# Optimization experiments

Measured on AMD Instinct MI355X. Metric: run time of the kernel, lower is better.

The kernel has to match this reference:

```python
import jax, jax.numpy as jnp
import numpy as np

LOW_THRESH = 0.3   # below -> background (label 0)
HIGH_THRESH = 0.7  # at/above -> foreground (label 1); in-between -> ignore (-1)


def _make_boxes(key, n):
    # two random corners per box -> valid (y1,x1,y2,x2) via min/max
    c = jax.random.uniform(key, (n, 2, 2), dtype=jnp.float32)
    lo = jnp.min(c, axis=1)
    hi = jnp.max(c, axis=1)
    return jnp.concatenate([lo, hi], axis=-1)  # [n, 4] = (y1, x1, y2, x2)


def setup_inputs() -> dict:
    key = jax.random.key(0)
    k1, k2 = jax.random.split(key)
    boxes1 = _make_boxes(k1, 262144)  # anchors / proposals
    boxes2 = _make_boxes(k2, 128)     # ground-truth boxes
    return {"boxes1": boxes1, "boxes2": boxes2}


def pairwise_iou(boxes1, boxes2):
    # boxes: (y1, x1, y2, x2). Result: [N1, N2]
    area1 = (boxes1[:, 2] - boxes1[:, 0]) * (boxes1[:, 3] - boxes1[:, 1])  # [N1]
    area2 = (boxes2[:, 2] - boxes2[:, 0]) * (boxes2[:, 3] - boxes2[:, 1])  # [N2]
    # intersection corners, broadcast [N1,1] vs [N2]
    iy1 = jnp.maximum(boxes1[:, None, 0], boxes2[None, :, 0])
    ix1 = jnp.maximum(boxes1[:, None, 1], boxes2[None, :, 1])
    iy2 = jnp.minimum(boxes1[:, None, 2], boxes2[None, :, 2])
    ix2 = jnp.minimum(boxes1[:, None, 3], boxes2[None, :, 3])
    inter = jnp.maximum(iy2 - iy1, 0.0) * jnp.maximum(ix2 - ix1, 0.0)  # [N1, N2]
    union = area1[:, None] + area2[None, :] - inter
    return inter / jnp.maximum(union, 1e-10)


def reference(boxes1, boxes2):
    iou = pairwise_iou(boxes1, boxes2)          # [N1, N2]
    matched_vals = jnp.max(iou, axis=1)         # [N1] best IoU per anchor
    matched_idx = jnp.argmax(iou, axis=1)       # [N1] index of best gt box
    labels = jnp.where(
        matched_vals >= HIGH_THRESH,
        jnp.int32(1),
        jnp.where(matched_vals < LOW_THRESH, jnp.int32(0), jnp.int32(-1)),
    )
    return matched_vals, matched_idx, labels
```

## Files before the change

### kernel.cpp

```cpp
#include <hip/hip_runtime.h>

#define N2 128
#define BLOCK 256

__global__ __launch_bounds__(BLOCK) void matcher_kernel(
    const float4* __restrict__ boxes1,
    const float4* __restrict__ boxes2,
    float* __restrict__ out_vals,
    float* __restrict__ out_idx,
    float* __restrict__ out_labels,
    int n1)
{
#pragma clang fp contract(off)
    __shared__ float4 s_b2[N2];
    __shared__ float s_area2[N2];

    const int t = threadIdx.x;
    if (t < N2) {
        float4 b = boxes2[t];
        s_b2[t] = b;
        s_area2[t] = (b.z - b.x) * (b.w - b.y);
    }
    __syncthreads();

    const int i = blockIdx.x * BLOCK + t;
    if (i >= n1) return;

    const float4 a = boxes1[i];
    const float area1 = (a.z - a.x) * (a.w - a.y);

    float best = -1.0f;
    int bidx = 0;

#pragma unroll 4
    for (int j = 0; j < N2; ++j) {
        const float4 b = s_b2[j];
        const float iy1 = fmaxf(a.x, b.x);
        const float ix1 = fmaxf(a.y, b.y);
        const float iy2 = fminf(a.z, b.z);
        const float ix2 = fminf(a.w, b.w);
        const float hy = fmaxf(iy2 - iy1, 0.0f);
        const float hx = fmaxf(ix2 - ix1, 0.0f);
        const float inter = hy * hx;
        const float uni = (area1 + s_area2[j]) - inter;
        const float iou = inter / fmaxf(uni, 1e-10f);
        if (iou > best) { best = iou; bidx = j; }
    }

    out_vals[i]   = best;
    out_idx[i]    = (float)bidx;
    out_labels[i] = (best >= 0.7f) ? 1.0f : ((best < 0.3f) ? 0.0f : -1.0f);
}

extern "C" void kernel_launch(void* const* d_in, const int* in_sizes, int n_in,
                              void* d_out, int out_size, void* d_ws, size_t ws_size,
                              hipStream_t stream) {
    const float4* boxes1 = (const float4*)d_in[0];
    const float4* boxes2 = (const float4*)d_in[1];
    const int n1 = in_sizes[0] / 4;

    float* out = (float*)d_out;
    float* out_vals   = out;
    float* out_idx    = out + n1;
    float* out_labels = out + 2 * n1;

    const int grid = (n1 + BLOCK - 1) / BLOCK;
    matcher_kernel<<<grid, BLOCK, 0, stream>>>(boxes1, boxes2,
                                               out_vals, out_idx, out_labels, n1);
}
```

Measured before the change: 31.70 us.

## Replace per-pair division with cross-multiplied IoU comparison and exact fallback

Instead of dividing inter by union for every pair, the kernel keeps the best (inter, union) fraction and compares candidates by cross-multiplication, doing a single division at the end. Two independent running maxima over the halves of the GT boxes shorten the dependency chain. When a comparison lands within a rounding tolerance band, a flag forces an exact recomputation with divisions so argmax ties and rounding match the reference. This adds extra multiplies and comparisons and a divergent slow path for near-ties.

```diff
diff --git a/kernel.cpp b/kernel.cpp
--- a/kernel.cpp
+++ b/kernel.cpp
@@ -2,6 +2,9 @@
 
 #define N2 128
 #define BLOCK 256
+
+#define ONE_P 1.00000095367431640625f
+#define ONE_M 0.99999904632568359375f
 
 __global__ __launch_bounds__(BLOCK) void matcher_kernel(
     const float4* __restrict__ boxes1,
@@ -29,27 +32,77 @@
     const float4 a = boxes1[i];
     const float area1 = (a.z - a.x) * (a.w - a.y);
 
-    float best = -1.0f;
-    int bidx = 0;
+    float biA = -1.0f, buA = 1.0f; int bxA = 0;
+    float biB = -1.0f, buB = 1.0f; int bxB = 64;
+    bool slow = false;
+
+#define FRAC(J, INTER, UM)                                            \
+    {                                                                 \
+        const float4 b = s_b2[(J)];                                   \
+        const float iy1 = fmaxf(a.x, b.x);                            \
+        const float ix1 = fmaxf(a.y, b.y);                            \
+        const float iy2 = fminf(a.z, b.z);                            \
+        const float ix2 = fminf(a.w, b.w);                            \
+        const float hy = fmaxf(iy2 - iy1, 0.0f);                      \
+        const float hx = fmaxf(ix2 - ix1, 0.0f);                      \
+        INTER = hy * hx;                                              \
+        UM = fmaxf((area1 + s_area2[(J)]) - INTER, 1e-10f);           \
+    }
+
+#define STEP(BI, BU, BX, INTER, UM, J)                                \
+    {                                                                 \
+        const float p1 = (INTER) * (BU);                              \
+        const float p2 = (BI) * (UM);                                 \
+        const float p2p = p2 * ONE_P;                                 \
+        const float p2m = p2 * ONE_M;                                 \
+        const bool upd = p1 > p2p;                                    \
+        slow = slow | (((INTER) > 0.0f) & (p1 >= p2m) & (p1 <= p2p)); \
+        if (upd) { BI = (INTER); BU = (UM); BX = (J); }               \
+    }
 
 #pragma unroll 4
-    for (int j = 0; j < N2; ++j) {
-        const float4 b = s_b2[j];
-        const float iy1 = fmaxf(a.x, b.x);
-        const float ix1 = fmaxf(a.y, b.y);
-        const float iy2 = fminf(a.z, b.z);
-        const float ix2 = fminf(a.w, b.w);
-        const float hy = fmaxf(iy2 - iy1, 0.0f);
-        const float hx = fmaxf(ix2 - ix1, 0.0f);
-        const float inter = hy * hx;
-        const float uni = (area1 + s_area2[j]) - inter;
-        const float iou = inter / fmaxf(uni, 1e-10f);
-        if (iou > best) { best = iou; bidx = j; }
+    for (int j = 0; j < 64; ++j) {
+        {
+            float inter, um;
+            FRAC(j, inter, um)
+            STEP(biA, buA, bxA, inter, um, j)
+        }
+        {
+            float inter, um;
+            FRAC(j + 64, inter, um)
+            STEP(biB, buB, bxB, inter, um, j + 64)
+        }
     }
 
-    out_vals[i]   = best;
-    out_idx[i]    = (float)bidx;
-    out_labels[i] = (best >= 0.7f) ? 1.0f : ((best < 0.3f) ? 0.0f : -1.0f);
+    {
+        const float p1 = biB * buA;
+        const float p2 = biA * buB;
+        const float p2p = p2 * ONE_P;
+        const float p2m = p2 * ONE_M;
+        const bool upd = p1 > p2p;
+        slow = slow | ((biB > 0.0f) & (p1 >= p2m) & (p1 <= p2p));
+        if (upd) { biA = biB; buA = buB; bxA = bxB; }
+    }
+
+    float d = biA / buA;
+    int xi = bxA;
+
+    if (slow) {
+        float best = -1.0f;
+        int bidx = 0;
+        for (int j = 0; j < N2; ++j) {
+            float inter, um;
+            FRAC(j, inter, um)
+            const float q = inter / um;
+            if (q > best) { best = q; bidx = j; }
+        }
+        d = best;
+        xi = bidx;
+    }
+
+    out_vals[i]   = d;
+    out_idx[i]    = (float)xi;
+    out_labels[i] = (d >= 0.7f) ? 1.0f : ((d < 0.3f) ? 0.0f : -1.0f);
 }
 
 extern "C" void kernel_launch(void* const* d_in, const int* in_sizes, int n_in,
```

After: 40.24 us. +26.9%, slower.

## Split gt-box loop across four wavefronts per anchor group and reduce in LDS

Applied to the files above, without the earlier changes.

Each block now handles 64 anchors, with each of its four wavefronts scanning 32 of the 128 ground-truth boxes. The partial argmax results are merged through shared memory. The gt box coordinates are read via wave-uniform global (scalar) loads instead of LDS, and launch bounds request more occupancy. The grid is four times larger, and the split adds a barrier plus a serial merge in one wavefront. Tie-breaking still keeps the first index, because waves are merged in ascending order with a strict greater-than.

```diff
diff --git a/kernel.cpp b/kernel.cpp
--- a/kernel.cpp
+++ b/kernel.cpp
@@ -2,8 +2,9 @@
 
 #define N2 128
 #define BLOCK 256
+#define APB 64
 
-__global__ __launch_bounds__(BLOCK) void matcher_kernel(
+__global__ __launch_bounds__(BLOCK, 8) void matcher_kernel(
     const float4* __restrict__ boxes1,
     const float4* __restrict__ boxes2,
     float* __restrict__ out_vals,
@@ -12,29 +13,34 @@
     int n1)
 {
 #pragma clang fp contract(off)
-    __shared__ float4 s_b2[N2];
     __shared__ float s_area2[N2];
+    __shared__ float s_q[4][APB];
+    __shared__ int   s_ix[4][APB];
 
     const int t = threadIdx.x;
     if (t < N2) {
-        float4 b = boxes2[t];
-        s_b2[t] = b;
+        const float4 b = boxes2[t];
         s_area2[t] = (b.z - b.x) * (b.w - b.y);
     }
     __syncthreads();
 
-    const int i = blockIdx.x * BLOCK + t;
-    if (i >= n1) return;
+    const int w    = __builtin_amdgcn_readfirstlane(t >> 6);
+    const int lane = t & 63;
+    const int i    = blockIdx.x * APB + lane;
+    const bool valid = (i < n1);
 
-    const float4 a = boxes1[i];
+    const float4 a = boxes1[valid ? i : 0];
     const float area1 = (a.z - a.x) * (a.w - a.y);
 
     float best = -1.0f;
-    int bidx = 0;
+    int   bidx = 0;
 
-#pragma unroll 4
-    for (int j = 0; j < N2; ++j) {
-        const float4 b = s_b2[j];
+    const int j0 = w * 32;
+#pragma unroll 8
+    for (int k = 0; k < 32; ++k) {
+        const int j = j0 + k;
+        const float4 b = boxes2[j];
+        const float a2 = s_area2[j];
         const float iy1 = fmaxf(a.x, b.x);
         const float ix1 = fmaxf(a.y, b.y);
         const float iy2 = fminf(a.z, b.z);
@@ -42,14 +48,30 @@
         const float hy = fmaxf(iy2 - iy1, 0.0f);
         const float hx = fmaxf(ix2 - ix1, 0.0f);
         const float inter = hy * hx;
-        const float uni = (area1 + s_area2[j]) - inter;
-        const float iou = inter / fmaxf(uni, 1e-10f);
-        if (iou > best) { best = iou; bidx = j; }
+        const float uni = (area1 + a2) - inter;
+        const float q = inter / fmaxf(uni, 1e-10f);
+        if (q > best) { best = q; bidx = j; }
     }
 
-    out_vals[i]   = best;
-    out_idx[i]    = (float)bidx;
-    out_labels[i] = (best >= 0.7f) ? 1.0f : ((best < 0.3f) ? 0.0f : -1.0f);
+    s_q[w][lane]  = best;
+    s_ix[w][lane] = bidx;
+    __syncthreads();
+
+    if (t < APB) {
+        const int ii = blockIdx.x * APB + t;
+        if (ii < n1) {
+            float q  = s_q[0][t];
+            int   ix = s_ix[0][t];
+#pragma unroll
+            for (int w2 = 1; w2 < 4; ++w2) {
+                const float q2 = s_q[w2][t];
+                if (q2 > q) { q = q2; ix = s_ix[w2][t]; }
+            }
+            out_vals[ii]   = q;
+            out_idx[ii]    = (float)ix;
+            out_labels[ii] = (q >= 0.7f) ? 1.0f : ((q < 0.3f) ? 0.0f : -1.0f);
+        }
+    }
 }
 
 extern "C" void kernel_launch(void* const* d_in, const int* in_sizes, int n_in,
@@ -64,7 +86,7 @@
     float* out_idx    = out + n1;
     float* out_labels = out + 2 * n1;
 
-    const int grid = (n1 + BLOCK - 1) / BLOCK;
+    const int grid = (n1 + APB - 1) / APB;
     matcher_kernel<<<grid, BLOCK, 0, stream>>>(boxes1, boxes2,
                                                out_vals, out_idx, out_labels, n1);
 }
```

Result: faster. 29.02 us (-8.5%).

## Use fast reciprocal IoU scan with top-2 tracking and exact fallback

Applied to the files above, without the earlier changes.

Replaces the per-pair IEEE division with a hardware approximate reciprocal and tracks the top two IoU values across two interleaved 64-wide chains. When the top two are within a relative band, it reruns the exact division scan so the argmax stays correct, then recomputes the winning IoU exactly for output. Ground-truth boxes are now read through uniform global loads instead of shared memory, and a launch-bounds occupancy hint is added. The cost is extra registers and a divergent fallback path for near-ties, with first-index tie-breaking handled through the fallback.

```diff
diff --git a/kernel.cpp b/kernel.cpp
--- a/kernel.cpp
+++ b/kernel.cpp
@@ -2,8 +2,9 @@
 
 #define N2 128
 #define BLOCK 256
+#define BAND 9.5367431640625e-07f
 
-__global__ __launch_bounds__(BLOCK) void matcher_kernel(
+__global__ __launch_bounds__(BLOCK, 8) void matcher_kernel(
     const float4* __restrict__ boxes1,
     const float4* __restrict__ boxes2,
     float* __restrict__ out_vals,
@@ -12,44 +13,87 @@
     int n1)
 {
 #pragma clang fp contract(off)
-    __shared__ float4 s_b2[N2];
     __shared__ float s_area2[N2];
 
     const int t = threadIdx.x;
     if (t < N2) {
-        float4 b = boxes2[t];
-        s_b2[t] = b;
+        const float4 b = boxes2[t];
         s_area2[t] = (b.z - b.x) * (b.w - b.y);
     }
     __syncthreads();
 
     const int i = blockIdx.x * BLOCK + t;
-    if (i >= n1) return;
-
-    const float4 a = boxes1[i];
+    const float4 a = boxes1[(i < n1) ? i : 0];
     const float area1 = (a.z - a.x) * (a.w - a.y);
 
-    float best = -1.0f;
-    int bidx = 0;
+    float bqA = -1.0f, b2A = -1.0f; int ixA = 0;
+    float bqB = -1.0f, b2B = -1.0f; int ixB = 0;
 
 #pragma unroll 4
-    for (int j = 0; j < N2; ++j) {
-        const float4 b = s_b2[j];
-        const float iy1 = fmaxf(a.x, b.x);
-        const float ix1 = fmaxf(a.y, b.y);
-        const float iy2 = fminf(a.z, b.z);
-        const float ix2 = fminf(a.w, b.w);
-        const float hy = fmaxf(iy2 - iy1, 0.0f);
-        const float hx = fmaxf(ix2 - ix1, 0.0f);
-        const float inter = hy * hx;
-        const float uni = (area1 + s_area2[j]) - inter;
-        const float iou = inter / fmaxf(uni, 1e-10f);
-        if (iou > best) { best = iou; bidx = j; }
+    for (int k = 0; k < 64; ++k) {
+        {
+            const float4 b = boxes2[k];
+            const float a2 = s_area2[k];
+            const float hy = fmaxf(fminf(a.z, b.z) - fmaxf(a.x, b.x), 0.0f);
+            const float hx = fmaxf(fminf(a.w, b.w) - fmaxf(a.y, b.y), 0.0f);
+            const float inter = hy * hx;
+            const float um = fmaxf((area1 + a2) - inter, 1e-10f);
+            const float q = inter * __builtin_amdgcn_rcpf(um);
+            b2A = fmaxf(b2A, fminf(bqA, q));
+            const bool cc = q > bqA;
+            bqA = fmaxf(bqA, q);
+            ixA = cc ? k : ixA;
+        }
+        {
+            const float4 b = boxes2[k + 64];
+            const float a2 = s_area2[k + 64];
+            const float hy = fmaxf(fminf(a.z, b.z) - fmaxf(a.x, b.x), 0.0f);
+            const float hx = fmaxf(fminf(a.w, b.w) - fmaxf(a.y, b.y), 0.0f);
+            const float inter = hy * hx;
+            const float um = fmaxf((area1 + a2) - inter, 1e-10f);
+            const float q = inter * __builtin_amdgcn_rcpf(um);
+            b2B = fmaxf(b2B, fminf(bqB, q));
+            const bool cc = q > bqB;
+            bqB = fmaxf(bqB, q);
+            ixB = cc ? k : ixB;
+        }
     }
 
-    out_vals[i]   = best;
-    out_idx[i]    = (float)bidx;
-    out_labels[i] = (best >= 0.7f) ? 1.0f : ((best < 0.3f) ? 0.0f : -1.0f);
+    const float top = fmaxf(bqA, bqB);
+    const float sec = fmaxf(fminf(bqA, bqB), fmaxf(b2A, b2B));
+    int bidx = (bqB > bqA) ? (ixB + 64) : ixA;
+
+    const bool slow = (top > 0.0f) && ((top - sec) <= top * BAND);
+
+    if (slow) {
+        float best = -1.0f;
+        int   bx = 0;
+        for (int j = 0; j < N2; ++j) {
+            const float4 b = boxes2[j];
+            const float a2 = s_area2[j];
+            const float hy = fmaxf(fminf(a.z, b.z) - fmaxf(a.x, b.x), 0.0f);
+            const float hx = fmaxf(fminf(a.w, b.w) - fmaxf(a.y, b.y), 0.0f);
+            const float inter = hy * hx;
+            const float um = fmaxf((area1 + a2) - inter, 1e-10f);
+            const float qq = inter / um;
+            if (qq > best) { best = qq; bx = j; }
+        }
+        bidx = bx;
+    }
+
+    const float4 wb = boxes2[bidx];
+    const float wa2 = (wb.z - wb.x) * (wb.w - wb.y);
+    const float why = fmaxf(fminf(a.z, wb.z) - fmaxf(a.x, wb.x), 0.0f);
+    const float whx = fmaxf(fminf(a.w, wb.w) - fmaxf(a.y, wb.y), 0.0f);
+    const float winter = why * whx;
+    const float wum = fmaxf((area1 + wa2) - winter, 1e-10f);
+    const float qe = winter / wum;
+
+    if (i < n1) {
+        out_vals[i]   = qe;
+        out_idx[i]    = (float)bidx;
+        out_labels[i] = (qe >= 0.7f) ? 1.0f : ((qe < 0.3f) ? 0.0f : -1.0f);
+    }
 }
 
 extern "C" void kernel_launch(void* const* d_in, const int* in_sizes, int n_in,
```

After: 37.39 us. 1.18x slower.
